# Optimization experiments

Hardware: AMD Instinct MI355X
Metric: run time of the kernel (lower is better)

The kernel has to match this reference:

```python
import jax, jax.numpy as jnp
import numpy as np

NUM_HEADS = 20
MAX_SEQLEN = 1500  # max per-segment length (Whisper 30s -> 1500 frames); static for jit
NEG = -1e30


def setup_inputs() -> dict:
    key = jax.random.key(0)
    ks = jax.random.split(key, 6)
    B, S, D = 4, MAX_SEQLEN, 1280
    T = B * S
    hidden_states = jax.random.normal(ks[0], (T, D), dtype=jnp.float32)
    # packed varlen layout: 4 equal-length audio segments
    cu_seqlens = (jnp.arange(B + 1, dtype=jnp.int32) * S)
    w = 0.02
    Wq = jax.random.normal(ks[1], (D, D), dtype=jnp.float32) * w
    Wk = jax.random.normal(ks[2], (D, D), dtype=jnp.float32) * w
    Wv = jax.random.normal(ks[3], (D, D), dtype=jnp.float32) * w
    Wo = jax.random.normal(ks[4], (D, D), dtype=jnp.float32) * w
    bq = jnp.zeros((D,), jnp.float32)
    bv = jnp.zeros((D,), jnp.float32)
    bo = jnp.zeros((D,), jnp.float32)
    return {"hidden_states": hidden_states, "cu_seqlens": cu_seqlens,
            "Wq": Wq, "bq": bq, "Wk": Wk, "Wv": Wv, "bv": bv, "Wo": Wo, "bo": bo}


def _varlen_attention(hidden_states, cu_seqlens, Wq, bq, Wk, Wv, bv, Wo, bo):
    T, D = hidden_states.shape
    H = NUM_HEADS
    d = D // H
    scale = d ** -0.5
    S = MAX_SEQLEN
    B = cu_seqlens.shape[0] - 1

    # projections (torch nn.Linear convention: y = x @ W.T + b; k_proj has no bias)
    q = hidden_states @ Wq.T + bq   # [T, D]
    k = hidden_states @ Wk.T        # [T, D]
    v = hidden_states @ Wv.T + bv   # [T, D]

    lens = cu_seqlens[1:] - cu_seqlens[:-1]                 # [B]
    pos = jnp.arange(S, dtype=jnp.int32)                    # [S]
    valid = pos[None, :] < lens[:, None]                    # [B, S]
    idx = cu_seqlens[:-1, None] + pos[None, :]              # [B, S]
    idx_g = jnp.where(valid, idx, 0)

    # unpack to padded [B, S, H, d]
    qb = q[idx_g].reshape(B, S, H, d)
    kb = k[idx_g].reshape(B, S, H, d)
    vb = v[idx_g].reshape(B, S, H, d)

    scores = jnp.einsum('bqhd,bkhd->bhqk', qb, kb) * scale  # [B, H, S, S]
    scores = jnp.where(valid[:, None, None, :], scores, NEG)
    attn = jax.nn.softmax(scores, axis=-1)
    out = jnp.einsum('bhqk,bkhd->bqhd', attn, vb).reshape(B, S, D)

    # repack to [T, D]; invalid slots scatter out-of-bounds and are dropped
    idx_s = jnp.where(valid, idx, T).reshape(-1)
    packed = jnp.zeros((T, D), out.dtype).at[idx_s].set(out.reshape(-1, D), mode='drop')
    return packed @ Wo.T + bo


def reference(hidden_states, cu_seqlens, Wq, bq, Wk, Wv, bv, Wo, bo):
    return _varlen_attention(hidden_states, cu_seqlens, Wq, bq, Wk, Wv, bv, Wo, bo)
```

## Files before the change

### kernel.cpp

```cpp
#include <hip/hip_runtime.h>
#include <stdint.h>
#include <math.h>

#define DMODEL 1280
#define NHEAD  20
#define DHEAD  64
#define NSEG   4
#define MAXS   1500
#define SPAD   1536
#define TPAD   (NSEG*SPAD)
#define QT128  ((MAXS + 127) / 128)
#define BM 128
#define BN 128
#define BK 32
#define QSCALE 0.18033688011112042f
#define NEGV  -1e30f

typedef float  f32x4  __attribute__((ext_vector_type(4)));
typedef __bf16 bf16x8 __attribute__((ext_vector_type(8)));

#if __has_builtin(__builtin_amdgcn_exp2f)
#define EXP2F(x) __builtin_amdgcn_exp2f(x)
#else
#define EXP2F(x) exp2f(x)
#endif

__device__ __forceinline__ ushort f2bf(float f) {
  union { float f; uint32_t u; } a; a.f = f;
  uint32_t u = a.u;
  u += 0x7FFFu + ((u >> 16) & 1u);
  return (ushort)(u >> 16);
}

__device__ __forceinline__ uint32_t pk2(float a, float b) {
  union { float f; uint32_t u; } ua, ub; ua.f = a; ub.f = b;
  uint32_t x = ua.u + 0x8000u, y = ub.u + 0x8000u;
  return (x >> 16) | (y & 0xFFFF0000u);
}

__device__ __forceinline__ void async16(const void* g, void* lds) {
  __builtin_amdgcn_global_load_lds((const __attribute__((address_space(1))) void*)g,
                                   (__attribute__((address_space(3))) void*)lds,
                                   16, 0, 0);
}

__device__ __forceinline__ int perm32(int a) {
  return ((a >> 2) & 3) * 8 + ((a >> 4) & 1) * 4 + (a & 3);
}

__global__ void __launch_bounds__(256)
cvt_all(const float* __restrict__ hs, const float* __restrict__ Wq,
        const float* __restrict__ Wk, const float* __restrict__ Wv,
        const float* __restrict__ Wo, ushort* __restrict__ dst, int nX, int DD) {
  const int i = (blockIdx.x * 256 + threadIdx.x) * 4;
  const float* src;
  if (i < nX) {
    src = hs + i;
  } else {
    int j = i - nX;
    const int z = (j >= DD) + (j >= 2 * DD) + (j >= 3 * DD);
    const float* w = (z == 0) ? Wq : (z == 1) ? Wk : (z == 2) ? Wv : Wo;
    src = w + (j - z * DD);
  }
  float4 v = *(const float4*)src;
  ushort4 o;
  o.x = f2bf(v.x); o.y = f2bf(v.y); o.z = f2bf(v.z); o.w = f2bf(v.w);
  *(ushort4*)(dst + i) = o;
}

__device__ __forceinline__ void gemm_tile_mainloop(
    const ushort* __restrict__ A, const ushort* __restrict__ W,
    int M, int m0, int n0, ushort* As, ushort* Bs, f32x4 (&acc)[4][4])
{
  const int tid  = threadIdx.x;
  const int wave = tid >> 6, lane = tid & 63;
  const int quad = lane >> 4, c16 = lane & 15;
  const int wr = (wave >> 1) * 64, wc = (wave & 1) * 64;

  const int M0 = wave * 128 + lane, M1 = M0 + 64;
  const int sr0 = M0 >> 3, pp0 = M0 & 7, p0 = pp0 ^ (sr0 & 7);
  const int sr1 = M1 >> 3, pp1 = M1 & 7, p1 = pp1 ^ (sr1 & 7);
  const int row0 = sr0 * 2 + (p0 >> 2), kc0 = (p0 & 3) << 3;
  const int row1 = sr1 * 2 + (p1 >> 2), kc1 = (p1 & 3) << 3;
  const ushort* Ap0 = A + (size_t)(m0 + row0) * DMODEL + kc0;
  const ushort* Ap1 = A + (size_t)(m0 + row1) * DMODEL + kc1;
  const ushort* Bp0 = W + (size_t)(n0 + row0) * DMODEL + kc0;
  const ushort* Bp1 = W + (size_t)(n0 + row1) * DMODEL + kc1;
  const int o0 = wave * 1024;
  const int o1 = wave * 1024 + 512;
  const int BUF = BM * BK;

  async16(Ap0, As + o0); async16(Ap1, As + o1);
  async16(Bp0, Bs + o0); async16(Bp1, Bs + o1);

  int c = 0;
  for (int k0 = 0; k0 < DMODEL; k0 += BK, c ^= 1) {
    __syncthreads();
    if (k0 + BK < DMODEL) {
      const int kn = k0 + BK;
      const int bo = (c ^ 1) * BUF;
      async16(Ap0 + kn, As + bo + o0); async16(Ap1 + kn, As + bo + o1);
      async16(Bp0 + kn, Bs + bo + o0); async16(Bp1 + kn, Bs + bo + o1);
    }
    const ushort* Ab = As + c * BUF;
    const ushort* Bb = Bs + c * BUF;
    bf16x8 a[4], b[4];
#pragma unroll
    for (int i = 0; i < 4; ++i) {
      const int row = wr + i * 16 + c16;
      const int sr = row >> 1;
      const int off = (sr << 6) + (((((row & 1) << 2) | quad) ^ (sr & 7)) << 3);
      a[i] = *(const bf16x8*)(Ab + off);
    }
#pragma unroll
    for (int j = 0; j < 4; ++j) {
      const int row = wc + j * 16 + c16;
      const int sr = row >> 1;
      const int off = (sr << 6) + (((((row & 1) << 2) | quad) ^ (sr & 7)) << 3);
      b[j] = *(const bf16x8*)(Bb + off);
    }
#pragma unroll
    for (int i = 0; i < 4; ++i)
#pragma unroll
      for (int j = 0; j < 4; ++j)
        acc[i][j] = __builtin_amdgcn_mfma_f32_16x16x32_bf16(a[i], b[j], acc[i][j], 0, 0, 0);
  }
}

__global__ void __launch_bounds__(256, 4)
gemm_qkv(const ushort* __restrict__ X, const ushort* __restrict__ W4,
         const float* __restrict__ bq, const float* __restrict__ bv,
         const int* __restrict__ cu,
         ushort* __restrict__ qb, ushort* __restrict__ kb, ushort* __restrict__ vt, int M)
{
  __shared__ ushort As[2 * BM * BK], Bs[2 * BN * BK];
  const int wg = blockIdx.x;
  if (wg >= 30) return;
  const int z = wg / 10;
  const int n0 = (wg % 10) * BN;
  const int m0 = blockIdx.y * BM;
  const ushort* W = W4 + (size_t)z * DMODEL * DMODEL;

  f32x4 acc[4][4];
  f32x4 zero = {0.f, 0.f, 0.f, 0.f};
#pragma unroll
  for (int i = 0; i < 4; ++i)
#pragma unroll
    for (int j = 0; j < 4; ++j) acc[i][j] = zero;

  gemm_tile_mainloop(X, W, M, m0, n0, As, Bs, acc);

  const int tid = threadIdx.x, wave = tid >> 6, lane = tid & 63;
  const int quad = lane >> 4, c16 = lane & 15;
  const int wr = (wave >> 1) * 64, wc = (wave & 1) * 64;

  if (z == 2) {
    const int c1 = cu[1], c2 = cu[2], c3 = cu[3];
#pragma unroll
    for (int i = 0; i < 4; ++i) {
      const int t0 = m0 + wr + i * 16 + quad * 4;
      const int s0a = (t0 >= c1) + (t0 >= c2) + (t0 >= c3);
      const int s3a = (t0 + 3 >= c1) + (t0 + 3 >= c2) + (t0 + 3 >= c3);
      const int seg0 = (s0a == 0) ? 0 : (s0a == 1) ? c1 : (s0a == 2) ? c2 : c3;
#pragma unroll
      for (int j = 0; j < 4; ++j) {
        const int cfeat = n0 + wc + j * 16 + c16;
        const float bb = bv[cfeat];
        if (t0 + 3 < M && s0a == s3a) {
          const int s = t0 - seg0;
          const size_t base = (size_t)cfeat * TPAD + (size_t)s0a * SPAD
                            + (size_t)(s & ~31) + perm32(s & 31);
          ushort4 w;
          w.x = f2bf(acc[i][j][0] + bb);
          w.y = f2bf(acc[i][j][1] + bb);
          w.z = f2bf(acc[i][j][2] + bb);
          w.w = f2bf(acc[i][j][3] + bb);
          *(ushort4*)(vt + base) = w;
        } else {
#pragma unroll
          for (int r = 0; r < 4; ++r) {
            const int t = t0 + r;
            if (t < M) {
              const int sb = (t >= c1) + (t >= c2) + (t >= c3);
              const int sg = (sb == 0) ? 0 : (sb == 1) ? c1 : (sb == 2) ? c2 : c3;
              const int s = t - sg;
              vt[(size_t)cfeat * TPAD + (size_t)sb * SPAD + (s & ~31) + perm32(s & 31)]
                  = f2bf(acc[i][j][r] + bb);
            }
          }
        }
      }
    }
  } else {
    ushort* out = (z == 0) ? qb : kb;
    const float* bias = (z == 0) ? bq : (const float*)nullptr;
    const float oscale = (z == 0) ? QSCALE : 1.0f;
#pragma unroll
    for (int i = 0; i < 4; ++i) {
      const int rbase = m0 + wr + i * 16 + quad * 4;
#pragma unroll
      for (int j = 0; j < 4; ++j) {
        const int c = n0 + wc + j * 16 + c16;
        const float bb = bias ? bias[c] : 0.f;
#pragma unroll
        for (int r = 0; r < 4; ++r) {
          const int rr = rbase + r;
          if (rr < M) out[(size_t)rr * DMODEL + c] = f2bf((acc[i][j][r] + bb) * oscale);
        }
      }
    }
  }
}

__global__ void __launch_bounds__(256, 4)
gemm_out(const ushort* __restrict__ A, const ushort* __restrict__ W,
         const float* __restrict__ bias, float* __restrict__ out, int M)
{
  __shared__ ushort As[2 * BM * BK], Bs[2 * BN * BK];
  const int wg = blockIdx.x;
  if (wg >= 10) return;
  const int n0 = wg * BN;
  const int m0 = blockIdx.y * BM;
  f32x4 acc[4][4];
  f32x4 zero = {0.f, 0.f, 0.f, 0.f};
#pragma unroll
  for (int i = 0; i < 4; ++i)
#pragma unroll
    for (int j = 0; j < 4; ++j) acc[i][j] = zero;

  gemm_tile_mainloop(A, W, M, m0, n0, As, Bs, acc);

  const int tid = threadIdx.x, wave = tid >> 6, lane = tid & 63;
  const int quad = lane >> 4, c16 = lane & 15;
  const int wr = (wave >> 1) * 64, wc = (wave & 1) * 64;
#pragma unroll
  for (int i = 0; i < 4; ++i) {
    const int rbase = m0 + wr + i * 16 + quad * 4;
#pragma unroll
    for (int j = 0; j < 4; ++j) {
      const int c = n0 + wc + j * 16 + c16;
      const float bb = bias[c];
#pragma unroll
      for (int r = 0; r < 4; ++r) {
        const int rr = rbase + r;
        if (rr < M) out[(size_t)rr * DMODEL + c] = acc[i][j][r] + bb;
      }
    }
  }
}

__global__ void __launch_bounds__(256, 4)
attn_fused(const ushort* __restrict__ qb, const ushort* __restrict__ kb,
           const ushort* __restrict__ vt, ushort* __restrict__ ob,
           const int* __restrict__ cu, int T)
{
  __shared__ ushort SB[2][8192];
  const int hs = blockIdx.x;
  const int b = hs / NHEAD, h = hs % NHEAD;
  const int seg0 = cu[b];
  const int len  = cu[b + 1] - seg0;
  const int q0 = blockIdx.y * 128;
  if (q0 >= len) return;
  const int tid = threadIdx.x, wave = tid >> 6, lane = tid & 63;
  const int quad = lane >> 4, c16 = lane & 15;

  {
    const int s = wave * 64 + lane;
#pragma unroll
    for (int t = 0; t < 4; ++t) {
      const int slot = t * 256 + s;
      const int r = slot >> 3, k2 = slot & 7;
      const int col = ((k2 ^ (r & 7)) << 3);
      async16(qb + (size_t)(seg0 + q0 + r) * DMODEL + h * DHEAD + col,
              &SB[0][(t * 256 + wave * 64) * 8]);
    }
  }

  const int sl  = wave * 64 + lane;
  const int rr0 = sl >> 3, kk2 = sl & 7;
  const int colc = ((kk2 ^ (rr0 & 7)) << 3);
  const ushort* kp0 = kb + (size_t)(seg0 + rr0) * DMODEL + h * DHEAD + colc;
  const ushort* kp1 = kp0 + (size_t)32 * DMODEL;
  const ushort* vp0 = vt + (size_t)(h * DHEAD + rr0) * TPAD + (size_t)b * SPAD + colc;
  const ushort* vp1 = vp0 + (size_t)32 * TPAD;
  const int ldo0 = wave * 512;
  const int ldo1 = 2048 + wave * 512;

  __syncthreads();

  bf16x8 aq[2][2];
#pragma unroll
  for (int n = 0; n < 2; ++n)
#pragma unroll
    for (int ks = 0; ks < 2; ++ks) {
      const int row = wave * 32 + n * 16 + c16;
      aq[n][ks] = *(const bf16x8*)(&SB[0][row * 64 + (((ks * 4 + quad) ^ (c16 & 7)) << 3)]);
    }

  async16(kp0, &SB[1][ldo0]);        async16(kp1, &SB[1][ldo1]);
  async16(vp0, &SB[1][4096 + ldo0]); async16(vp1, &SB[1][4096 + ldo1]);
  kp0 += (size_t)64 * DMODEL; kp1 += (size_t)64 * DMODEL; vp0 += 64; vp1 += 64;

  float l_i[2] = {0.f, 0.f};
  f32x4 o_acc[2][4];
  f32x4 zero = {0.f, 0.f, 0.f, 0.f};
#pragma unroll
  for (int n = 0; n < 2; ++n)
#pragma unroll
    for (int m = 0; m < 4; ++m) o_acc[n][m] = zero;

  const int niter = (len + 63) >> 6;
  for (int it = 0; it < niter; ++it) {
    __syncthreads();
    const ushort* Kt = &SB[1 ^ (it & 1)][0];
    const ushort* Vt = &SB[1 ^ (it & 1)][4096];

    if (it + 1 < niter) {
      ushort* Dst = &SB[it & 1][0];
      async16(kp0, Dst + ldo0);        async16(kp1, Dst + ldo1);
      async16(vp0, Dst + 4096 + ldo0); async16(vp1, Dst + 4096 + ldo1);
      kp0 += (size_t)64 * DMODEL; kp1 += (size_t)64 * DMODEL; vp0 += 64; vp1 += 64;
    }

    f32x4 s[2][4];
#pragma unroll
    for (int f = 0; f < 4; ++f) {
      const int row = f * 16 + c16;
      const int ch = c16 & 7;
      bf16x8 ak0 = *(const bf16x8*)(Kt + row * 64 + ((quad ^ ch) << 3));
      bf16x8 ak1 = *(const bf16x8*)(Kt + row * 64 + (((4 + quad) ^ ch) << 3));
#pragma unroll
      for (int n = 0; n < 2; ++n) {
        s[n][f] = zero;
        s[n][f] = __builtin_amdgcn_mfma_f32_16x16x32_bf16(ak0, aq[n][0], s[n][f], 0, 0, 0);
        s[n][f] = __builtin_amdgcn_mfma_f32_16x16x32_bf16(ak1, aq[n][1], s[n][f], 0, 0, 0);
      }
    }

    const int kv0 = it * 64;
    if (kv0 + 64 > len) {
#pragma unroll
      for (int f = 0; f < 4; ++f) {
        const int kvb = kv0 + f * 16 + quad * 4;
#pragma unroll
        for (int r = 0; r < 4; ++r)
          if (kvb + r >= len) { s[0][f][r] = NEGV; s[1][f][r] = NEGV; }
      }
    }

#pragma unroll
    for (int n = 0; n < 2; ++n) {
      float rs = 0.f;
#pragma unroll
      for (int f = 0; f < 4; ++f)
#pragma unroll
        for (int r = 0; r < 4; ++r) {
          const float p = EXP2F(s[n][f][r]);
          s[n][f][r] = p;
          rs += p;
        }
      l_i[n] += rs;
    }

    bf16x8 bp[2][2];
#pragma unroll
    for (int n = 0; n < 2; ++n)
#pragma unroll
      for (int g = 0; g < 2; ++g) {
        union { uint32_t u[4]; bf16x8 v; } cv;
        cv.u[0] = pk2(s[n][2 * g][0], s[n][2 * g][1]);
        cv.u[1] = pk2(s[n][2 * g][2], s[n][2 * g][3]);
        cv.u[2] = pk2(s[n][2 * g + 1][0], s[n][2 * g + 1][1]);
        cv.u[3] = pk2(s[n][2 * g + 1][2], s[n][2 * g + 1][3]);
        bp[n][g] = cv.v;
      }

#pragma unroll
    for (int m = 0; m < 4; ++m) {
      const int row = m * 16 + c16;
      const int ch = c16 & 7;
      bf16x8 av0 = *(const bf16x8*)(Vt + row * 64 + ((quad ^ ch) << 3));
      bf16x8 av1 = *(const bf16x8*)(Vt + row * 64 + (((4 + quad) ^ ch) << 3));
#pragma unroll
      for (int n = 0; n < 2; ++n) {
        o_acc[n][m] = __builtin_amdgcn_mfma_f32_16x16x32_bf16(av0, bp[n][0], o_acc[n][m], 0, 0, 0);
        o_acc[n][m] = __builtin_amdgcn_mfma_f32_16x16x32_bf16(av1, bp[n][1], o_acc[n][m], 0, 0, 0);
      }
    }
  }

#pragma unroll
  for (int n = 0; n < 2; ++n) {
    float l = l_i[n];
    l += __shfl_xor(l, 16);
    l += __shfl_xor(l, 32);
    const int q = q0 + wave * 32 + n * 16 + c16;
    if (q < len) {
      const float inv = 1.0f / l;
      const size_t base = (size_t)(seg0 + q) * DMODEL + h * DHEAD;
#pragma unroll
      for (int m = 0; m < 4; ++m) {
        ushort4 pk;
        pk.x = f2bf(o_acc[n][m][0] * inv);
        pk.y = f2bf(o_acc[n][m][1] * inv);
        pk.z = f2bf(o_acc[n][m][2] * inv);
        pk.w = f2bf(o_acc[n][m][3] * inv);
        *(ushort4*)(ob + base + m * 16 + quad * 4) = pk;
      }
    }
  }
}

extern "C" void kernel_launch(void* const* d_in, const int* in_sizes, int n_in,
                              void* d_out, int out_size, void* d_ws, size_t ws_size,
                              hipStream_t stream)
{
  (void)n_in; (void)out_size; (void)ws_size;
  const float* hs = (const float*)d_in[0];
  const int*   cu = (const int*)d_in[1];
  const float* Wq = (const float*)d_in[2];
  const float* bq = (const float*)d_in[3];
  const float* Wk = (const float*)d_in[4];
  const float* Wv = (const float*)d_in[5];
  const float* bv = (const float*)d_in[6];
  const float* Wo = (const float*)d_in[7];
  const float* bo = (const float*)d_in[8];
  float* out = (float*)d_out;
  const int T  = in_sizes[0] / DMODEL;
  const int DD = DMODEL * DMODEL;
  const int nX = T * DMODEL;

  ushort* ws  = (ushort*)d_ws;
  ushort* X   = ws;
  ushort* W4  = X + (size_t)nX;
  ushort* qb  = W4 + 4 * (size_t)DD;
  ushort* kb  = qb + (size_t)T * DMODEL;
  ushort* vt  = kb + (size_t)T * DMODEL;
  ushort* ob  = X;

  const int ncvt = nX + 4 * DD;
  cvt_all<<<(ncvt / 4 + 255) / 256, 256, 0, stream>>>(hs, Wq, Wk, Wv, Wo, ws, nX, DD);

  gemm_qkv<<<dim3(32, (T + BM - 1) / BM), 256, 0, stream>>>(
      X, W4, bq, bv, cu, qb, kb, vt, T);

  attn_fused<<<dim3(NSEG * NHEAD, QT128), 256, 0, stream>>>(qb, kb, vt, ob, cu, T);

  gemm_out<<<dim3(16, (T + BM - 1) / BM), 256, 0, stream>>>(
      ob, W4 + 3 * (size_t)DD, bo, out, T);
}
```

Measured before the change: 306.5 us.

## Enlarge projection GEMM tiles to 128x256 with 8 waves and XCD-aware block mapping

Replaces the 128x128x32 GEMM mainloop used by the QKV and output projections with a 128x256 tile, BK=64, and 512-thread blocks. Global-to-LDS staging now uses explicit vmcnt waits and raw barriers, and MFMA sections are wrapped in setprio. Blocks are launched on a 1D grid and remapped so that consecutive M tiles of the same N slice land on the same XCD, aiming to improve L2 reuse of weights and cut per-tile load overhead. In exchange it uses more LDS and fewer resident blocks per CU, and there are fewer blocks to balance across CUs.

```diff
diff --git a/kernel.cpp b/kernel.cpp
--- a/kernel.cpp
+++ b/kernel.cpp
@@ -11,8 +11,9 @@
 #define TPAD   (NSEG*SPAD)
 #define QT128  ((MAXS + 127) / 128)
 #define BM 128
-#define BN 128
-#define BK 32
+#define BN 256
+#define BK2 64
+#define NKT (DMODEL / BK2)
 #define QSCALE 0.18033688011112042f
 #define NEGV  -1e30f
 
@@ -47,6 +48,16 @@
 __device__ __forceinline__ int perm32(int a) {
   return ((a >> 2) & 3) * 8 + ((a >> 4) & 1) * 4 + (a & 3);
 }
+
+__device__ __forceinline__ int xcd_chunk(int d, int nwg) {
+  const int q = nwg >> 3, r = nwg & 7;
+  const int x = d & 7, pos = d >> 3;
+  return (x < r ? x * (q + 1) : r * (q + 1) + (x - r) * q) + pos;
+}
+
+#define GBAR()  do { asm volatile("" ::: "memory"); __builtin_amdgcn_s_barrier(); \
+                     asm volatile("" ::: "memory"); } while (0)
+#define WAITV(n) asm volatile("s_waitcnt vmcnt(" #n ")" ::: "memory")
 
 __global__ void __launch_bounds__(256)
 cvt_all(const float* __restrict__ hs, const float* __restrict__ Wq,
@@ -68,77 +79,107 @@
   *(ushort4*)(dst + i) = o;
 }
 
-__device__ __forceinline__ void gemm_tile_mainloop(
+__device__ __forceinline__ void do_phase(const ushort* Aks, const ushort* Bks,
+                                         const int (&offA)[4], const int (&offB)[4],
+                                         f32x4 (&acc)[4][4]) {
+  bf16x8 a[4], b[4];
+#pragma unroll
+  for (int i = 0; i < 4; ++i) a[i] = *(const bf16x8*)(Aks + offA[i]);
+#pragma unroll
+  for (int j = 0; j < 4; ++j) b[j] = *(const bf16x8*)(Bks + offB[j]);
+  __builtin_amdgcn_s_setprio(1);
+#pragma unroll
+  for (int i = 0; i < 4; ++i)
+#pragma unroll
+    for (int j = 0; j < 4; ++j)
+      acc[i][j] = __builtin_amdgcn_mfma_f32_16x16x32_bf16(a[i], b[j], acc[i][j], 0, 0, 0);
+  __builtin_amdgcn_s_setprio(0);
+}
+
+__device__ __forceinline__ void gemm256_mainloop(
     const ushort* __restrict__ A, const ushort* __restrict__ W,
-    int M, int m0, int n0, ushort* As, ushort* Bs, f32x4 (&acc)[4][4])
+    int m0, int n0, ushort* As, ushort* Bs, f32x4 (&acc)[4][4])
 {
-  const int tid  = threadIdx.x;
+  const int tid = threadIdx.x;
   const int wave = tid >> 6, lane = tid & 63;
   const int quad = lane >> 4, c16 = lane & 15;
-  const int wr = (wave >> 1) * 64, wc = (wave & 1) * 64;
-
-  const int M0 = wave * 128 + lane, M1 = M0 + 64;
-  const int sr0 = M0 >> 3, pp0 = M0 & 7, p0 = pp0 ^ (sr0 & 7);
-  const int sr1 = M1 >> 3, pp1 = M1 & 7, p1 = pp1 ^ (sr1 & 7);
-  const int row0 = sr0 * 2 + (p0 >> 2), kc0 = (p0 & 3) << 3;
-  const int row1 = sr1 * 2 + (p1 >> 2), kc1 = (p1 & 3) << 3;
-  const ushort* Ap0 = A + (size_t)(m0 + row0) * DMODEL + kc0;
-  const ushort* Ap1 = A + (size_t)(m0 + row1) * DMODEL + kc1;
-  const ushort* Bp0 = W + (size_t)(n0 + row0) * DMODEL + kc0;
-  const ushort* Bp1 = W + (size_t)(n0 + row1) * DMODEL + kc1;
-  const int o0 = wave * 1024;
-  const int o1 = wave * 1024 + 512;
-  const int BUF = BM * BK;
-
-  async16(Ap0, As + o0); async16(Ap1, As + o1);
-  async16(Bp0, Bs + o0); async16(Bp1, Bs + o1);
-
-  int c = 0;
-  for (int k0 = 0; k0 < DMODEL; k0 += BK, c ^= 1) {
-    __syncthreads();
-    if (k0 + BK < DMODEL) {
-      const int kn = k0 + BK;
-      const int bo = (c ^ 1) * BUF;
-      async16(Ap0 + kn, As + bo + o0); async16(Ap1 + kn, As + bo + o1);
-      async16(Bp0 + kn, Bs + bo + o0); async16(Bp1 + kn, Bs + bo + o1);
-    }
-    const ushort* Ab = As + c * BUF;
-    const ushort* Bb = Bs + c * BUF;
-    bf16x8 a[4], b[4];
-#pragma unroll
-    for (int i = 0; i < 4; ++i) {
-      const int row = wr + i * 16 + c16;
-      const int sr = row >> 1;
-      const int off = (sr << 6) + (((((row & 1) << 2) | quad) ^ (sr & 7)) << 3);
-      a[i] = *(const bf16x8*)(Ab + off);
-    }
-#pragma unroll
-    for (int j = 0; j < 4; ++j) {
-      const int row = wc + j * 16 + c16;
-      const int sr = row >> 1;
-      const int off = (sr << 6) + (((((row & 1) << 2) | quad) ^ (sr & 7)) << 3);
-      b[j] = *(const bf16x8*)(Bb + off);
-    }
-#pragma unroll
-    for (int i = 0; i < 4; ++i)
-#pragma unroll
-      for (int j = 0; j < 4; ++j)
-        acc[i][j] = __builtin_amdgcn_mfma_f32_16x16x32_bf16(a[i], b[j], acc[i][j], 0, 0, 0);
-  }
-}
-
-__global__ void __launch_bounds__(256, 4)
+  const int wr = (wave >> 2) * 64, wc = (wave & 3) * 64;
+  const int wofs = wave * 512;
+
+  const int sA = tid;
+  const int srA = sA >> 3, pA = (sA & 7) ^ (srA & 7);
+  const int rowA = srA * 2 + (pA >> 2), kcA = (pA & 3) << 3;
+  const int sB = tid + 512;
+  const int srB = sB >> 3, pB = (sB & 7) ^ (srB & 7);
+  const int rowB = srB * 2 + (pB >> 2), kcB = (pB & 3) << 3;
+
+  const ushort* Ap  = A + (size_t)(m0 + rowA) * DMODEL + kcA;
+  const ushort* Bp0 = W + (size_t)(n0 + rowA) * DMODEL + kcA;
+  const ushort* Bp1 = W + (size_t)(n0 + rowB) * DMODEL + kcB;
+
+  int offA[4], offB[4];
+#pragma unroll
+  for (int i = 0; i < 4; ++i) {
+    const int row = wr + i * 16 + c16, sr = row >> 1;
+    offA[i] = (sr << 6) + (((((row & 1) << 2) | quad) ^ (sr & 7)) << 3);
+  }
+#pragma unroll
+  for (int j = 0; j < 4; ++j) {
+    const int row = wc + j * 16 + c16, sr = row >> 1;
+    offB[j] = (sr << 6) + (((((row & 1) << 2) | quad) ^ (sr & 7)) << 3);
+  }
+
+#define STAGE(buf, kk) do { \
+    ushort* Ad = As + (buf) * 8192; \
+    ushort* Bd = Bs + (buf) * 16384; \
+    async16(Ap  + (kk),      Ad + wofs); \
+    async16(Ap  + (kk) + 32, Ad + 4096 + wofs); \
+    async16(Bp0 + (kk),      Bd + wofs); \
+    async16(Bp1 + (kk),      Bd + 4096 + wofs); \
+    async16(Bp0 + (kk) + 32, Bd + 8192 + wofs); \
+    async16(Bp1 + (kk) + 32, Bd + 8192 + 4096 + wofs); \
+  } while (0)
+
+  STAGE(0, 0);
+  STAGE(1, BK2);
+  WAITV(6);
+  GBAR();
+
+#pragma unroll 1
+  for (int t = 0; t < NKT; t += 2) {
+    do_phase(As, Bs, offA, offB, acc);
+    GBAR();
+    do_phase(As + 4096, Bs + 8192, offA, offB, acc);
+    if (t + 2 < NKT) { STAGE(0, (t + 2) * BK2); WAITV(6); }
+    else             { WAITV(0); }
+    GBAR();
+    do_phase(As + 8192, Bs + 16384, offA, offB, acc);
+    GBAR();
+    do_phase(As + 8192 + 4096, Bs + 16384 + 8192, offA, offB, acc);
+    if (t + 2 < NKT) {
+      if (t + 3 < NKT) { STAGE(1, (t + 3) * BK2); WAITV(6); }
+      else             { WAITV(0); }
+      GBAR();
+    }
+  }
+#undef STAGE
+}
+
+__global__ void __launch_bounds__(512, 2)
 gemm_qkv(const ushort* __restrict__ X, const ushort* __restrict__ W4,
          const float* __restrict__ bq, const float* __restrict__ bv,
          const int* __restrict__ cu,
-         ushort* __restrict__ qb, ushort* __restrict__ kb, ushort* __restrict__ vt, int M)
+         ushort* __restrict__ qb, ushort* __restrict__ kb, ushort* __restrict__ vt,
+         int M, int MT)
 {
-  __shared__ ushort As[2 * BM * BK], Bs[2 * BN * BK];
-  const int wg = blockIdx.x;
-  if (wg >= 30) return;
-  const int z = wg / 10;
-  const int n0 = (wg % 10) * BN;
-  const int m0 = blockIdx.y * BM;
+  __shared__ __align__(16) ushort As[2 * BM * BK2];
+  __shared__ __align__(16) ushort Bs[2 * BN * BK2];
+  const int nwg = 15 * MT;
+  const int lid = xcd_chunk(blockIdx.x, nwg);
+  const int g = lid / MT, mt = lid - g * MT;
+  const int z = g / 5;
+  const int n0 = (g - z * 5) * BN;
+  const int m0 = mt * BM;
   const ushort* W = W4 + (size_t)z * DMODEL * DMODEL;
 
   f32x4 acc[4][4];
@@ -148,11 +189,11 @@
 #pragma unroll
     for (int j = 0; j < 4; ++j) acc[i][j] = zero;
 
-  gemm_tile_mainloop(X, W, M, m0, n0, As, Bs, acc);
+  gemm256_mainloop(X, W, m0, n0, As, Bs, acc);
 
   const int tid = threadIdx.x, wave = tid >> 6, lane = tid & 63;
   const int quad = lane >> 4, c16 = lane & 15;
-  const int wr = (wave >> 1) * 64, wc = (wave & 1) * 64;
+  const int wr = (wave >> 2) * 64, wc = (wave & 3) * 64;
 
   if (z == 2) {
     const int c1 = cu[1], c2 = cu[2], c3 = cu[3];
@@ -212,15 +253,18 @@
   }
 }
 
-__global__ void __launch_bounds__(256, 4)
+__global__ void __launch_bounds__(512, 2)
 gemm_out(const ushort* __restrict__ A, const ushort* __restrict__ W,
-         const float* __restrict__ bias, float* __restrict__ out, int M)
+         const float* __restrict__ bias, float* __restrict__ out, int M, int MT)
 {
-  __shared__ ushort As[2 * BM * BK], Bs[2 * BN * BK];
-  const int wg = blockIdx.x;
-  if (wg >= 10) return;
-  const int n0 = wg * BN;
-  const int m0 = blockIdx.y * BM;
+  __shared__ __align__(16) ushort As[2 * BM * BK2];
+  __shared__ __align__(16) ushort Bs[2 * BN * BK2];
+  const int nwg = 5 * MT;
+  const int lid = xcd_chunk(blockIdx.x, nwg);
+  const int g = lid / MT, mt = lid - g * MT;
+  const int n0 = g * BN;
+  const int m0 = mt * BM;
+
   f32x4 acc[4][4];
   f32x4 zero = {0.f, 0.f, 0.f, 0.f};
 #pragma unroll
@@ -228,11 +272,11 @@
 #pragma unroll
     for (int j = 0; j < 4; ++j) acc[i][j] = zero;
 
-  gemm_tile_mainloop(A, W, M, m0, n0, As, Bs, acc);
+  gemm256_mainloop(A, W, m0, n0, As, Bs, acc);
 
   const int tid = threadIdx.x, wave = tid >> 6, lane = tid & 63;
   const int quad = lane >> 4, c16 = lane & 15;
-  const int wr = (wave >> 1) * 64, wc = (wave & 1) * 64;
+  const int wr = (wave >> 2) * 64, wc = (wave & 3) * 64;
 #pragma unroll
   for (int i = 0; i < 4; ++i) {
     const int rbase = m0 + wr + i * 16 + quad * 4;
@@ -429,6 +473,7 @@
   const int T  = in_sizes[0] / DMODEL;
   const int DD = DMODEL * DMODEL;
   const int nX = T * DMODEL;
+  const int MT = (T + BM - 1) / BM;
 
   ushort* ws  = (ushort*)d_ws;
   ushort* X   = ws;
@@ -441,11 +486,9 @@
   const int ncvt = nX + 4 * DD;
   cvt_all<<<(ncvt / 4 + 255) / 256, 256, 0, stream>>>(hs, Wq, Wk, Wv, Wo, ws, nX, DD);
 
-  gemm_qkv<<<dim3(32, (T + BM - 1) / BM), 256, 0, stream>>>(
-      X, W4, bq, bv, cu, qb, kb, vt, T);
+  gemm_qkv<<<15 * MT, 512, 0, stream>>>(X, W4, bq, bv, cu, qb, kb, vt, T, MT);
 
   attn_fused<<<dim3(NSEG * NHEAD, QT128), 256, 0, stream>>>(qb, kb, vt, ob, cu, T);
 
-  gemm_out<<<dim3(16, (T + BM - 1) / BM), 256, 0, stream>>>(
-      ob, W4 + 3 * (size_t)DD, bo, out, T);
-}
+  gemm_out<<<5 * MT, 512, 0, stream>>>(ob, W4 + 3 * (size_t)DD, bo, out, T, MT);
+}
```

New measurement: 304.3 us. No clear change (-0.7%).

## Widen attention blocks to 256 query rows with 8 waves sharing K/V tiles

Applied to the files above, without the earlier changes.

The attention kernel now runs 512 threads per block covering 256 query rows, so each K/V tile in LDS is shared by eight waves instead of four. This halves the global K/V reloads per head and lets each thread issue one async load per tile instead of two. It also adds s_setprio around the MFMA sections to favour matrix issue across waves. The cost is fewer blocks in the grid (6 query tiles per head instead of 12) and more tail waste at length 1500, since the last tile covers only 220 of 256 rows.

```diff
diff --git a/kernel.cpp b/kernel.cpp
--- a/kernel.cpp
+++ b/kernel.cpp
@@ -9,7 +9,7 @@
 #define MAXS   1500
 #define SPAD   1536
 #define TPAD   (NSEG*SPAD)
-#define QT128  ((MAXS + 127) / 128)
+#define QT256  ((MAXS + 255) / 256)
 #define BM 128
 #define BN 128
 #define BK 32
@@ -249,42 +249,35 @@
   }
 }
 
-__global__ void __launch_bounds__(256, 4)
+__global__ void __launch_bounds__(512, 4)
 attn_fused(const ushort* __restrict__ qb, const ushort* __restrict__ kb,
            const ushort* __restrict__ vt, ushort* __restrict__ ob,
            const int* __restrict__ cu, int T)
 {
-  __shared__ ushort SB[2][8192];
+  __shared__ ushort SB[16384];
   const int hs = blockIdx.x;
   const int b = hs / NHEAD, h = hs % NHEAD;
   const int seg0 = cu[b];
   const int len  = cu[b + 1] - seg0;
-  const int q0 = blockIdx.y * 128;
+  const int q0 = blockIdx.y * 256;
   if (q0 >= len) return;
   const int tid = threadIdx.x, wave = tid >> 6, lane = tid & 63;
   const int quad = lane >> 4, c16 = lane & 15;
 
-  {
-    const int s = wave * 64 + lane;
-#pragma unroll
-    for (int t = 0; t < 4; ++t) {
-      const int slot = t * 256 + s;
-      const int r = slot >> 3, k2 = slot & 7;
-      const int col = ((k2 ^ (r & 7)) << 3);
-      async16(qb + (size_t)(seg0 + q0 + r) * DMODEL + h * DHEAD + col,
-              &SB[0][(t * 256 + wave * 64) * 8]);
-    }
-  }
-
-  const int sl  = wave * 64 + lane;
-  const int rr0 = sl >> 3, kk2 = sl & 7;
-  const int colc = ((kk2 ^ (rr0 & 7)) << 3);
-  const ushort* kp0 = kb + (size_t)(seg0 + rr0) * DMODEL + h * DHEAD + colc;
-  const ushort* kp1 = kp0 + (size_t)32 * DMODEL;
-  const ushort* vp0 = vt + (size_t)(h * DHEAD + rr0) * TPAD + (size_t)b * SPAD + colc;
-  const ushort* vp1 = vp0 + (size_t)32 * TPAD;
-  const int ldo0 = wave * 512;
-  const int ldo1 = 2048 + wave * 512;
+#pragma unroll
+  for (int t = 0; t < 4; ++t) {
+    const int slot = t * 512 + tid;
+    const int r = slot >> 3, k2 = slot & 7;
+    const int col = ((k2 ^ (r & 7)) << 3);
+    async16(qb + (size_t)(seg0 + q0 + r) * DMODEL + h * DHEAD + col,
+            &SB[(t * 512 + wave * 64) * 8]);
+  }
+
+  const int rK = tid >> 3, kK = tid & 7;
+  const int colK = ((kK ^ (rK & 7)) << 3);
+  const ushort* kp = kb + (size_t)(seg0 + rK) * DMODEL + h * DHEAD + colK;
+  const ushort* vp = vt + (size_t)(h * DHEAD + rK) * TPAD + (size_t)b * SPAD + colK;
+  const int ldsoff = wave * 512;
 
   __syncthreads();
 
@@ -294,12 +287,13 @@
 #pragma unroll
     for (int ks = 0; ks < 2; ++ks) {
       const int row = wave * 32 + n * 16 + c16;
-      aq[n][ks] = *(const bf16x8*)(&SB[0][row * 64 + (((ks * 4 + quad) ^ (c16 & 7)) << 3)]);
-    }
-
-  async16(kp0, &SB[1][ldo0]);        async16(kp1, &SB[1][ldo1]);
-  async16(vp0, &SB[1][4096 + ldo0]); async16(vp1, &SB[1][4096 + ldo1]);
-  kp0 += (size_t)64 * DMODEL; kp1 += (size_t)64 * DMODEL; vp0 += 64; vp1 += 64;
+      aq[n][ks] = *(const bf16x8*)(&SB[row * 64 + (((ks * 4 + quad) ^ (c16 & 7)) << 3)]);
+    }
+
+  __syncthreads();
+
+  async16(kp, &SB[ldsoff]); async16(vp, &SB[4096 + ldsoff]);
+  kp += (size_t)64 * DMODEL; vp += 64;
 
   float l_i[2] = {0.f, 0.f};
   f32x4 o_acc[2][4];
@@ -312,17 +306,17 @@
   const int niter = (len + 63) >> 6;
   for (int it = 0; it < niter; ++it) {
     __syncthreads();
-    const ushort* Kt = &SB[1 ^ (it & 1)][0];
-    const ushort* Vt = &SB[1 ^ (it & 1)][4096];
+    const ushort* Kt = &SB[(it & 1) * 8192];
+    const ushort* Vt = Kt + 4096;
 
     if (it + 1 < niter) {
-      ushort* Dst = &SB[it & 1][0];
-      async16(kp0, Dst + ldo0);        async16(kp1, Dst + ldo1);
-      async16(vp0, Dst + 4096 + ldo0); async16(vp1, Dst + 4096 + ldo1);
-      kp0 += (size_t)64 * DMODEL; kp1 += (size_t)64 * DMODEL; vp0 += 64; vp1 += 64;
+      ushort* Dst = &SB[((it + 1) & 1) * 8192];
+      async16(kp, Dst + ldsoff); async16(vp, Dst + 4096 + ldsoff);
+      kp += (size_t)64 * DMODEL; vp += 64;
     }
 
     f32x4 s[2][4];
+    __builtin_amdgcn_s_setprio(1);
 #pragma unroll
     for (int f = 0; f < 4; ++f) {
       const int row = f * 16 + c16;
@@ -336,6 +330,7 @@
         s[n][f] = __builtin_amdgcn_mfma_f32_16x16x32_bf16(ak1, aq[n][1], s[n][f], 0, 0, 0);
       }
     }
+    __builtin_amdgcn_s_setprio(0);
 
     const int kv0 = it * 64;
     if (kv0 + 64 > len) {
@@ -375,6 +370,7 @@
         bp[n][g] = cv.v;
       }
 
+    __builtin_amdgcn_s_setprio(1);
 #pragma unroll
     for (int m = 0; m < 4; ++m) {
       const int row = m * 16 + c16;
@@ -387,6 +383,7 @@
         o_acc[n][m] = __builtin_amdgcn_mfma_f32_16x16x32_bf16(av1, bp[n][1], o_acc[n][m], 0, 0, 0);
       }
     }
+    __builtin_amdgcn_s_setprio(0);
   }
 
 #pragma unroll
@@ -444,7 +441,7 @@
   gemm_qkv<<<dim3(32, (T + BM - 1) / BM), 256, 0, stream>>>(
       X, W4, bq, bv, cu, qb, kb, vt, T);
 
-  attn_fused<<<dim3(NSEG * NHEAD, QT128), 256, 0, stream>>>(qb, kb, vt, ob, cu, T);
+  attn_fused<<<dim3(NSEG * NHEAD, QT256), 512, 0, stream>>>(qb, kb, vt, ob, cu, T);
 
   gemm_out<<<dim3(16, (T + BM - 1) / BM), 256, 0, stream>>>(
       ob, W4 + 3 * (size_t)DD, bo, out, T);
```

Measured after the change: 303.3 us. Within noise of the previous version (-1.0%).

## Fuse all stages into one cooperative persistent kernel with grid syncs

Applied to the files above, without the earlier changes.

Replaces the four separate launches (convert, QKV GEMM, attention, output GEMM) with a single cooperative persistent kernel. Each stage loops over job indices and the stages are separated by grid.sync, with a fallback to separate launches if the cooperative launch fails. It also adds s_setprio around the MFMA blocks in attention and swaps the manual bf16 packing for native casts. This removes launch gaps and tail effects between kernels, at the cost of grid-wide barriers, a fixed grid of at most 1024 blocks, and a possible difference in rounding behaviour from the native casts.

```diff
diff --git a/kernel.cpp b/kernel.cpp
--- a/kernel.cpp
+++ b/kernel.cpp
@@ -1,6 +1,9 @@
 #include <hip/hip_runtime.h>
+#include <hip/hip_cooperative_groups.h>
 #include <stdint.h>
 #include <math.h>
+
+namespace cg = cooperative_groups;
 
 #define DMODEL 1280
 #define NHEAD  20
@@ -9,10 +12,12 @@
 #define MAXS   1500
 #define SPAD   1536
 #define TPAD   (NSEG*SPAD)
-#define QT128  ((MAXS + 127) / 128)
 #define BM 128
 #define BN 128
 #define BK 32
+#define NJ_QKV (30*47)
+#define NJ_ATTN (NSEG*NHEAD*12)
+#define NJ_OUT (10*47)
 #define QSCALE 0.18033688011112042f
 #define NEGV  -1e30f
 
@@ -32,12 +37,6 @@
   return (ushort)(u >> 16);
 }
 
-__device__ __forceinline__ uint32_t pk2(float a, float b) {
-  union { float f; uint32_t u; } ua, ub; ua.f = a; ub.f = b;
-  uint32_t x = ua.u + 0x8000u, y = ub.u + 0x8000u;
-  return (x >> 16) | (y & 0xFFFF0000u);
-}
-
 __device__ __forceinline__ void async16(const void* g, void* lds) {
   __builtin_amdgcn_global_load_lds((const __attribute__((address_space(1))) void*)g,
                                    (__attribute__((address_space(3))) void*)lds,
@@ -48,24 +47,33 @@
   return ((a >> 2) & 3) * 8 + ((a >> 4) & 1) * 4 + (a & 3);
 }
 
-__global__ void __launch_bounds__(256)
-cvt_all(const float* __restrict__ hs, const float* __restrict__ Wq,
-        const float* __restrict__ Wk, const float* __restrict__ Wv,
-        const float* __restrict__ Wo, ushort* __restrict__ dst, int nX, int DD) {
-  const int i = (blockIdx.x * 256 + threadIdx.x) * 4;
-  const float* src;
-  if (i < nX) {
-    src = hs + i;
-  } else {
-    int j = i - nX;
-    const int z = (j >= DD) + (j >= 2 * DD) + (j >= 3 * DD);
-    const float* w = (z == 0) ? Wq : (z == 1) ? Wk : (z == 2) ? Wv : Wo;
-    src = w + (j - z * DD);
-  }
-  float4 v = *(const float4*)src;
-  ushort4 o;
-  o.x = f2bf(v.x); o.y = f2bf(v.y); o.z = f2bf(v.z); o.w = f2bf(v.w);
-  *(ushort4*)(dst + i) = o;
+
+__device__ __forceinline__ void cvt_phase(
+    const float* __restrict__ hs, const float* __restrict__ Wq,
+    const float* __restrict__ Wk, const float* __restrict__ Wv,
+    const float* __restrict__ Wo, ushort* __restrict__ dst, int nX, int DD)
+{
+  const int ng = (nX + 4 * DD) >> 3;
+  const int stride = gridDim.x * 256;
+  for (int g = blockIdx.x * 256 + threadIdx.x; g < ng; g += stride) {
+    const int i = g << 3;
+    const float* src;
+    if (i < nX) {
+      src = hs + i;
+    } else {
+      const int j = i - nX;
+      const int z = (j >= DD) + (j >= 2 * DD) + (j >= 3 * DD);
+      const float* w = (z == 0) ? Wq : (z == 1) ? Wk : (z == 2) ? Wv : Wo;
+      src = w + (j - z * DD);
+    }
+    const float4 v0 = ((const float4*)src)[0];
+    const float4 v1 = ((const float4*)src)[1];
+    ushort4 o0, o1;
+    o0.x = f2bf(v0.x); o0.y = f2bf(v0.y); o0.z = f2bf(v0.z); o0.w = f2bf(v0.w);
+    o1.x = f2bf(v1.x); o1.y = f2bf(v1.y); o1.z = f2bf(v1.z); o1.w = f2bf(v1.w);
+    ((ushort4*)(dst + i))[0] = o0;
+    ((ushort4*)(dst + i))[1] = o1;
+  }
 }
 
 __device__ __forceinline__ void gemm_tile_mainloop(
@@ -127,18 +135,17 @@
   }
 }
 
-__global__ void __launch_bounds__(256, 4)
-gemm_qkv(const ushort* __restrict__ X, const ushort* __restrict__ W4,
-         const float* __restrict__ bq, const float* __restrict__ bv,
-         const int* __restrict__ cu,
-         ushort* __restrict__ qb, ushort* __restrict__ kb, ushort* __restrict__ vt, int M)
-{
-  __shared__ ushort As[2 * BM * BK], Bs[2 * BN * BK];
-  const int wg = blockIdx.x;
-  if (wg >= 30) return;
+__device__ __forceinline__ void qkv_job(
+    int job, const ushort* __restrict__ X, const ushort* __restrict__ W4,
+    const float* __restrict__ bq, const float* __restrict__ bv,
+    const int* __restrict__ cu,
+    ushort* __restrict__ qb, ushort* __restrict__ kb, ushort* __restrict__ vt,
+    int M, ushort* As, ushort* Bs)
+{
+  const int wg = job / 47, mt = job - wg * 47;
   const int z = wg / 10;
-  const int n0 = (wg % 10) * BN;
-  const int m0 = blockIdx.y * BM;
+  const int n0 = (wg - z * 10) * BN;
+  const int m0 = mt * BM;
   const ushort* W = W4 + (size_t)z * DMODEL * DMODEL;
 
   f32x4 acc[4][4];
@@ -212,57 +219,20 @@
   }
 }
 
-__global__ void __launch_bounds__(256, 4)
-gemm_out(const ushort* __restrict__ A, const ushort* __restrict__ W,
-         const float* __restrict__ bias, float* __restrict__ out, int M)
-{
-  __shared__ ushort As[2 * BM * BK], Bs[2 * BN * BK];
-  const int wg = blockIdx.x;
-  if (wg >= 10) return;
-  const int n0 = wg * BN;
-  const int m0 = blockIdx.y * BM;
-  f32x4 acc[4][4];
-  f32x4 zero = {0.f, 0.f, 0.f, 0.f};
-#pragma unroll
-  for (int i = 0; i < 4; ++i)
-#pragma unroll
-    for (int j = 0; j < 4; ++j) acc[i][j] = zero;
-
-  gemm_tile_mainloop(A, W, M, m0, n0, As, Bs, acc);
-
+__device__ __forceinline__ void attn_job(
+    int job, const ushort* __restrict__ qb, const ushort* __restrict__ kb,
+    const ushort* __restrict__ vt, ushort* __restrict__ ob,
+    const int* __restrict__ cu, ushort* SBf)
+{
+  const int qt = job / 80, hs = job - qt * 80;
+  const int b = hs / NHEAD, h = hs - b * NHEAD;
+  const int seg0 = cu[b];
+  const int len  = cu[b + 1] - seg0;
+  const int q0 = qt * 128;
   const int tid = threadIdx.x, wave = tid >> 6, lane = tid & 63;
   const int quad = lane >> 4, c16 = lane & 15;
-  const int wr = (wave >> 1) * 64, wc = (wave & 1) * 64;
-#pragma unroll
-  for (int i = 0; i < 4; ++i) {
-    const int rbase = m0 + wr + i * 16 + quad * 4;
-#pragma unroll
-    for (int j = 0; j < 4; ++j) {
-      const int c = n0 + wc + j * 16 + c16;
-      const float bb = bias[c];
-#pragma unroll
-      for (int r = 0; r < 4; ++r) {
-        const int rr = rbase + r;
-        if (rr < M) out[(size_t)rr * DMODEL + c] = acc[i][j][r] + bb;
-      }
-    }
-  }
-}
-
-__global__ void __launch_bounds__(256, 4)
-attn_fused(const ushort* __restrict__ qb, const ushort* __restrict__ kb,
-           const ushort* __restrict__ vt, ushort* __restrict__ ob,
-           const int* __restrict__ cu, int T)
-{
-  __shared__ ushort SB[2][8192];
-  const int hs = blockIdx.x;
-  const int b = hs / NHEAD, h = hs % NHEAD;
-  const int seg0 = cu[b];
-  const int len  = cu[b + 1] - seg0;
-  const int q0 = blockIdx.y * 128;
-  if (q0 >= len) return;
-  const int tid = threadIdx.x, wave = tid >> 6, lane = tid & 63;
-  const int quad = lane >> 4, c16 = lane & 15;
+
+  __syncthreads();
 
   {
     const int s = wave * 64 + lane;
@@ -272,7 +242,7 @@
       const int r = slot >> 3, k2 = slot & 7;
       const int col = ((k2 ^ (r & 7)) << 3);
       async16(qb + (size_t)(seg0 + q0 + r) * DMODEL + h * DHEAD + col,
-              &SB[0][(t * 256 + wave * 64) * 8]);
+              &SBf[(t * 256 + wave * 64) * 8]);
     }
   }
 
@@ -294,11 +264,13 @@
 #pragma unroll
     for (int ks = 0; ks < 2; ++ks) {
       const int row = wave * 32 + n * 16 + c16;
-      aq[n][ks] = *(const bf16x8*)(&SB[0][row * 64 + (((ks * 4 + quad) ^ (c16 & 7)) << 3)]);
-    }
-
-  async16(kp0, &SB[1][ldo0]);        async16(kp1, &SB[1][ldo1]);
-  async16(vp0, &SB[1][4096 + ldo0]); async16(vp1, &SB[1][4096 + ldo1]);
+      aq[n][ks] = *(const bf16x8*)(&SBf[row * 64 + (((ks * 4 + quad) ^ (c16 & 7)) << 3)]);
+    }
+
+  __syncthreads();
+
+  async16(kp0, &SBf[8192 + ldo0]);        async16(kp1, &SBf[8192 + ldo1]);
+  async16(vp0, &SBf[8192 + 4096 + ldo0]); async16(vp1, &SBf[8192 + 4096 + ldo1]);
   kp0 += (size_t)64 * DMODEL; kp1 += (size_t)64 * DMODEL; vp0 += 64; vp1 += 64;
 
   float l_i[2] = {0.f, 0.f};
@@ -312,17 +284,18 @@
   const int niter = (len + 63) >> 6;
   for (int it = 0; it < niter; ++it) {
     __syncthreads();
-    const ushort* Kt = &SB[1 ^ (it & 1)][0];
-    const ushort* Vt = &SB[1 ^ (it & 1)][4096];
+    const ushort* Kt = SBf + (1 ^ (it & 1)) * 8192;
+    const ushort* Vt = Kt + 4096;
 
     if (it + 1 < niter) {
-      ushort* Dst = &SB[it & 1][0];
+      ushort* Dst = SBf + (it & 1) * 8192;
       async16(kp0, Dst + ldo0);        async16(kp1, Dst + ldo1);
       async16(vp0, Dst + 4096 + ldo0); async16(vp1, Dst + 4096 + ldo1);
       kp0 += (size_t)64 * DMODEL; kp1 += (size_t)64 * DMODEL; vp0 += 64; vp1 += 64;
     }
 
     f32x4 s[2][4];
+    __builtin_amdgcn_s_setprio(1);
 #pragma unroll
     for (int f = 0; f < 4; ++f) {
       const int row = f * 16 + c16;
@@ -336,6 +309,7 @@
         s[n][f] = __builtin_amdgcn_mfma_f32_16x16x32_bf16(ak1, aq[n][1], s[n][f], 0, 0, 0);
       }
     }
+    __builtin_amdgcn_s_setprio(0);
 
     const int kv0 = it * 64;
     if (kv0 + 64 > len) {
@@ -367,14 +341,16 @@
     for (int n = 0; n < 2; ++n)
 #pragma unroll
       for (int g = 0; g < 2; ++g) {
-        union { uint32_t u[4]; bf16x8 v; } cv;
-        cv.u[0] = pk2(s[n][2 * g][0], s[n][2 * g][1]);
-        cv.u[1] = pk2(s[n][2 * g][2], s[n][2 * g][3]);
-        cv.u[2] = pk2(s[n][2 * g + 1][0], s[n][2 * g + 1][1]);
-        cv.u[3] = pk2(s[n][2 * g + 1][2], s[n][2 * g + 1][3]);
-        bp[n][g] = cv.v;
-      }
-
+        bf16x8 t;
+#pragma unroll
+        for (int r = 0; r < 4; ++r) {
+          t[r]     = (__bf16)s[n][2 * g][r];
+          t[r + 4] = (__bf16)s[n][2 * g + 1][r];
+        }
+        bp[n][g] = t;
+      }
+
+    __builtin_amdgcn_s_setprio(1);
 #pragma unroll
     for (int m = 0; m < 4; ++m) {
       const int row = m * 16 + c16;
@@ -387,6 +363,7 @@
         o_acc[n][m] = __builtin_amdgcn_mfma_f32_16x16x32_bf16(av1, bp[n][1], o_acc[n][m], 0, 0, 0);
       }
     }
+    __builtin_amdgcn_s_setprio(0);
   }
 
 #pragma unroll
@@ -409,6 +386,101 @@
       }
     }
   }
+}
+
+__device__ __forceinline__ void out_job(
+    int job, const ushort* __restrict__ A, const ushort* __restrict__ W,
+    const float* __restrict__ bias, float* __restrict__ out, int M,
+    ushort* As, ushort* Bs)
+{
+  const int nn = job / 47, mt = job - nn * 47;
+  const int n0 = nn * BN, m0 = mt * BM;
+  f32x4 acc[4][4];
+  f32x4 zero = {0.f, 0.f, 0.f, 0.f};
+#pragma unroll
+  for (int i = 0; i < 4; ++i)
+#pragma unroll
+    for (int j = 0; j < 4; ++j) acc[i][j] = zero;
+
+  gemm_tile_mainloop(A, W, M, m0, n0, As, Bs, acc);
+
+  const int tid = threadIdx.x, wave = tid >> 6, lane = tid & 63;
+  const int quad = lane >> 4, c16 = lane & 15;
+  const int wr = (wave >> 1) * 64, wc = (wave & 1) * 64;
+#pragma unroll
+  for (int i = 0; i < 4; ++i) {
+    const int rbase = m0 + wr + i * 16 + quad * 4;
+#pragma unroll
+    for (int j = 0; j < 4; ++j) {
+      const int c = n0 + wc + j * 16 + c16;
+      const float bb = bias[c];
+#pragma unroll
+      for (int r = 0; r < 4; ++r) {
+        const int rr = rbase + r;
+        if (rr < M) out[(size_t)rr * DMODEL + c] = acc[i][j][r] + bb;
+      }
+    }
+  }
+}
+
+struct MegaArgs {
+  const float *hs, *Wq, *Wk, *Wv, *Wo, *bq, *bv, *bo;
+  const int* cu;
+  float* out;
+  ushort *X, *W4, *qb, *kb, *vt;
+  int T, nX, DD;
+};
+
+__global__ void __launch_bounds__(256, 4)
+mega(MegaArgs a)
+{
+  cg::grid_group grid = cg::this_grid();
+  __shared__ __align__(16) ushort SB[16384];
+
+  cvt_phase(a.hs, a.Wq, a.Wk, a.Wv, a.Wo, a.X, a.nX, a.DD);
+  grid.sync();
+
+  for (int job = blockIdx.x; job < NJ_QKV; job += gridDim.x) {
+    __syncthreads();
+    qkv_job(job, a.X, a.W4, a.bq, a.bv, a.cu, a.qb, a.kb, a.vt, a.T, SB, SB + 8192);
+  }
+  grid.sync();
+
+  for (int job = blockIdx.x; job < NJ_ATTN; job += gridDim.x)
+    attn_job(job, a.qb, a.kb, a.vt, a.X , a.cu, SB);
+  grid.sync();
+
+  for (int job = blockIdx.x; job < NJ_OUT; job += gridDim.x) {
+    __syncthreads();
+    out_job(job, a.X , a.W4 + 3 * (size_t)a.DD, a.bo, a.out, a.T, SB, SB + 8192);
+  }
+}
+
+__global__ void __launch_bounds__(256)
+cvt_all_k(const float* hs, const float* Wq, const float* Wk, const float* Wv,
+          const float* Wo, ushort* dst, int nX, int DD) {
+  cvt_phase(hs, Wq, Wk, Wv, Wo, dst, nX, DD);
+}
+
+__global__ void __launch_bounds__(256, 4)
+gemm_qkv_k(const ushort* X, const ushort* W4, const float* bq, const float* bv,
+           const int* cu, ushort* qb, ushort* kb, ushort* vt, int M) {
+  __shared__ __align__(16) ushort SB[16384];
+  const int wg = blockIdx.x;
+  if (wg >= 30) return;
+  qkv_job(wg * 47 + blockIdx.y, X, W4, bq, bv, cu, qb, kb, vt, M, SB, SB + 8192);
+}
+
+__global__ void __launch_bounds__(256, 4)
+attn_k(const ushort* qb, const ushort* kb, const ushort* vt, ushort* ob, const int* cu) {
+  __shared__ __align__(16) ushort SB[16384];
+  attn_job(blockIdx.y * 80 + blockIdx.x, qb, kb, vt, ob, cu, SB);
+}
+
+__global__ void __launch_bounds__(256, 4)
+gemm_out_k(const ushort* A, const ushort* W, const float* bias, float* out, int M) {
+  __shared__ __align__(16) ushort SB[16384];
+  out_job(blockIdx.x * 47 + blockIdx.y, A, W, bias, out, M, SB, SB + 8192);
 }
 
 extern "C" void kernel_launch(void* const* d_in, const int* in_sizes, int n_in,
@@ -436,16 +508,31 @@
   ushort* qb  = W4 + 4 * (size_t)DD;
   ushort* kb  = qb + (size_t)T * DMODEL;
   ushort* vt  = kb + (size_t)T * DMODEL;
-  ushort* ob  = X;
-
-  const int ncvt = nX + 4 * DD;
-  cvt_all<<<(ncvt / 4 + 255) / 256, 256, 0, stream>>>(hs, Wq, Wk, Wv, Wo, ws, nX, DD);
-
-  gemm_qkv<<<dim3(32, (T + BM - 1) / BM), 256, 0, stream>>>(
-      X, W4, bq, bv, cu, qb, kb, vt, T);
-
-  attn_fused<<<dim3(NSEG * NHEAD, QT128), 256, 0, stream>>>(qb, kb, vt, ob, cu, T);
-
-  gemm_out<<<dim3(16, (T + BM - 1) / BM), 256, 0, stream>>>(
-      ob, W4 + 3 * (size_t)DD, bo, out, T);
-}
+
+  MegaArgs ma;
+  ma.hs = hs; ma.Wq = Wq; ma.Wk = Wk; ma.Wv = Wv; ma.Wo = Wo;
+  ma.bq = bq; ma.bv = bv; ma.bo = bo; ma.cu = cu; ma.out = out;
+  ma.X = X; ma.W4 = W4; ma.qb = qb; ma.kb = kb; ma.vt = vt;
+  ma.T = T; ma.nX = nX; ma.DD = DD;
+
+  int maxb = 0;
+  hipError_t oe = hipOccupancyMaxActiveBlocksPerMultiprocessor(&maxb, mega, 256, 0);
+  bool coop_done = false;
+  if (oe == hipSuccess && maxb >= 1) {
+    const int nb = (maxb < 4 ? maxb : 4) * 256;
+    void* args[] = { (void*)&ma };
+    hipError_t le = hipLaunchCooperativeKernel((const void*)mega, dim3(nb), dim3(256),
+                                               args, 0, stream);
+    if (le == hipSuccess) coop_done = true;
+    else (void)hipGetLastError();
+  } else {
+    (void)hipGetLastError();
+  }
+
+  if (!coop_done) {
+    cvt_all_k<<<2048, 256, 0, stream>>>(hs, Wq, Wk, Wv, Wo, ws, nX, DD);
+    gemm_qkv_k<<<dim3(32, 47), 256, 0, stream>>>(X, W4, bq, bv, cu, qb, kb, vt, T);
+    attn_k<<<dim3(80, 12), 256, 0, stream>>>(qb, kb, vt, X , cu);
+    gemm_out_k<<<dim3(10, 47), 256, 0, stream>>>(X , W4 + 3 * (size_t)DD, bo, out, T);
+  }
+}
```

New measurement: 533.1 us. +73.9%, slower.
